# Kernel optimization log

Measured on AMD Instinct MI355X. Metric: run time of the kernel, lower is better.

Reference implementation:

```python
import jax, jax.numpy as jnp
import numpy as np

B, T, E, H = 2, 2048, 1024, 16
D = E // H
K_KEEP = 391
RECENCY = 64
SCALE = D ** -0.5


def setup_inputs() -> dict:
    key = jax.random.key(0)
    k1, k2, k3 = jax.random.split(key, 3)
    x = jax.random.normal(k1, (B, T, E), jnp.float32)
    W_attn = jax.random.normal(k2, (3 * E, E), jnp.float32) * 0.02  # torch Linear weight [out,in]
    W_proj = jax.random.normal(k3, (E, E), jnp.float32) * 0.02
    return {"x": x, "W_attn": W_attn, "W_proj": W_proj}


def reference(x, W_attn, W_proj):
    b, t, c = x.shape
    qkv = x @ W_attn.T                      # [B,T,3E]
    q, k, v = jnp.split(qkv, 3, axis=-1)
    to_heads = lambda u: u.reshape(b, t, H, D).transpose(0, 2, 1, 3)  # [B,H,T,D]
    q, k, v = to_heads(q), to_heads(k), to_heads(v)

    # first pass: causal attention weights for importance scoring
    scores = jnp.einsum('bhqd,bhkd->bhqk', q, k) * SCALE
    causal = jnp.tril(jnp.ones((t, t), dtype=bool))
    scores = jnp.where(causal, scores, -jnp.inf)
    attn_w = jax.nn.softmax(scores, axis=-1)

    # mean importance over query dim, force-keep recent tokens
    imp = attn_w.mean(axis=2)               # [B,H,T]
    imp = imp.at[:, :, -RECENCY:].set(1.0)

    # top-k token selection per (batch, head)
    _, idx = jax.lax.top_k(imp, K_KEEP)     # [B,H,K]

    # gather pruned K/V
    K_keep = jnp.take_along_axis(k, idx[..., None], axis=2)  # [B,H,K,D]
    V_keep = jnp.take_along_axis(v, idx[..., None], axis=2)

    # second attention pass over pruned keys (no causal mask, matches legacy code)
    s2 = jnp.einsum('bhqd,bhkd->bhqk', q, K_keep) * SCALE
    a2 = jax.nn.softmax(s2, axis=-1)
    out = jnp.einsum('bhqk,bhkd->bhqd', a2, V_keep)          # [B,H,T,D]

    out = out.transpose(0, 2, 1, 3).reshape(b, t, c)
    return out @ W_proj.T
```

## Files before the change

kernel.cpp:

```cpp
#include <hip/hip_runtime.h>
#include <hip/hip_bf16.h>


#define TT 2048
#define EE 1024
#define HH 16
#define DD 64
#define KKEEP 391
#define REC 64
#define NBH 32
#define QSCALE 0.125f
#define KPAD 448

typedef short bf16x8 __attribute__((ext_vector_type(8)));
typedef _Float16 f16x8 __attribute__((ext_vector_type(8)));
typedef float f32x4 __attribute__((ext_vector_type(4)));

#define WAIT_VM(N) asm volatile("s_waitcnt vmcnt(" #N ")" ::: "memory")
#define WAIT_LGKM0 asm volatile("s_waitcnt lgkmcnt(0)" ::: "memory")
#define BAR() __builtin_amdgcn_s_barrier()

static __device__ inline unsigned short bf_rn(float x) {
  unsigned u = __float_as_uint(x);
  unsigned r = u + 0x7fffu + ((u >> 16) & 1u);
  return (unsigned short)(r >> 16);
}
static __device__ inline float bf_up(unsigned short h) {
  return __uint_as_float((unsigned)h << 16);
}
static __device__ inline unsigned pkf16(float a, float b) {
  union { _Float16 h[2]; unsigned u; } t;
  t.h[0] = (_Float16)a; t.h[1] = (_Float16)b; return t.u;
}
static __device__ inline void glds16(const void* g, void* l) {
  __builtin_amdgcn_global_load_lds(
      (const __attribute__((address_space(1))) void*)g,
      (__attribute__((address_space(3))) void*)l, 16, 0, 0);
}

static __device__ inline void split4(const float* __restrict__ src,
                                     unsigned short* __restrict__ ho,
                                     unsigned short* __restrict__ lo_, int i)
{
  float4 v = *reinterpret_cast<const float4*>(&src[i]);
  ushort4 hh, ll;
  float f;
  hh.x = bf_rn(v.x); f = bf_up(hh.x); ll.x = bf_rn(v.x - f);
  hh.y = bf_rn(v.y); f = bf_up(hh.y); ll.y = bf_rn(v.y - f);
  hh.z = bf_rn(v.z); f = bf_up(hh.z); ll.z = bf_rn(v.z - f);
  hh.w = bf_rn(v.w); f = bf_up(hh.w); ll.w = bf_rn(v.w - f);
  *reinterpret_cast<ushort4*>(&ho[i]) = hh;
  *reinterpret_cast<ushort4*>(&lo_[i]) = ll;
}

__global__ __launch_bounds__(256) void split_kernel(
    const float* __restrict__ src, unsigned short* __restrict__ ho,
    unsigned short* __restrict__ lo_, int n)
{
  int i = (blockIdx.x * 256 + threadIdx.x) * 4;
  const int stride = gridDim.x * 1024;
  for (; i < n; i += stride) split4(src, ho, lo_, i);
}

__global__ __launch_bounds__(256) void split2_kernel(
    const float* __restrict__ x, const float* __restrict__ wa,
    unsigned short* __restrict__ xh, unsigned short* __restrict__ xl,
    unsigned short* __restrict__ wh, unsigned short* __restrict__ wl)
{
  const int n1 = 4096 * 1024, n2 = 3072 * 1024;
  int i = (blockIdx.x * 256 + threadIdx.x) * 4;
  const int stride = gridDim.x * 1024;
  for (; i < n1 + n2; i += stride) {
    if (i < n1) split4(x, xh, xl, i);
    else        split4(wa, wh, wl, i - n1);
  }
}

template<bool VB, int MODE>
__global__ __launch_bounds__(256) void gemm_pipe(
    const unsigned short* __restrict__ Ah, const unsigned short* __restrict__ Al,
    const unsigned short* __restrict__ Bh, const unsigned short* __restrict__ Bl,
    float* __restrict__ Cc, unsigned short* __restrict__ Qho, unsigned short* __restrict__ Qlo,
    unsigned short* __restrict__ Kho, unsigned short* __restrict__ Klo,
    float* __restrict__ Vo, int M, int N, int Kd, int nOff)
{
  __shared__ __align__(16) unsigned short Ahs[2][128 * 32];
  __shared__ __align__(16) unsigned short Bhs[2][128 * 32];
  __shared__ __align__(16) unsigned short Als[VB ? 1 : 2][128 * 32];
  __shared__ __align__(16) unsigned short Bls[VB ? 1 : 2][128 * 32];
  const int tid = threadIdx.x;
  const int m0 = blockIdx.y * 128, n0 = nOff + blockIdx.x * 128;
  const int w = tid >> 6, lane = tid & 63;
  const int wm = w >> 1, wn = w & 1;
  const int l15 = lane & 15, l4 = lane >> 4;

  size_t gA[2], gB[2]; int ldso[2];
#pragma unroll
  for (int s = 0; s < 2; s++) {
    int seg = w * 2 + s;
    int r = seg * 16 + (lane >> 2);
    int kb = (lane & 3) ^ ((r >> 1) & 3);
    gA[s] = (size_t)(m0 + r) * Kd + kb * 8;
    gB[s] = (size_t)(n0 + r) * Kd + kb * 8;
    ldso[s] = seg * 512;
  }
  auto STAGE = [&](int bb, int k0) {
#pragma unroll
    for (int s = 0; s < 2; s++) {
      glds16(&Ah[gA[s] + k0], &Ahs[bb][ldso[s]]);
      glds16(&Bh[gB[s] + k0], &Bhs[bb][ldso[s]]);
      if (!VB) {
        glds16(&Al[gA[s] + k0], &Als[bb][ldso[s]]);
        glds16(&Bl[gB[s] + k0], &Bls[bb][ldso[s]]);
      }
    }
  };

  f32x4 acc[4][4] = {};

  STAGE(0, 0);
  STAGE(1, 32);
  int cur = 0;
  for (int k0 = 0; k0 < Kd; k0 += 32) {
    if (k0 + 32 < Kd) { if (VB) WAIT_VM(4); else WAIT_VM(8); }
    else WAIT_VM(0);
    BAR();
    bf16x8 ah[4], al[4], bh[4], bl[4];
#pragma unroll
    for (int i = 0; i < 4; i++) {
      int ar = wm * 64 + i * 16 + l15;
      int aoff = ar * 32 + ((l4 ^ ((ar >> 1) & 3)) * 8);
      ah[i] = *reinterpret_cast<const bf16x8*>(&Ahs[cur][aoff]);
      int br = wn * 64 + i * 16 + l15;
      int boff = br * 32 + ((l4 ^ ((br >> 1) & 3)) * 8);
      bh[i] = *reinterpret_cast<const bf16x8*>(&Bhs[cur][boff]);
      if (!VB) {
        al[i] = *reinterpret_cast<const bf16x8*>(&Als[cur][aoff]);
        bl[i] = *reinterpret_cast<const bf16x8*>(&Bls[cur][boff]);
      }
    }
#pragma unroll
    for (int i = 0; i < 4; i++)
#pragma unroll
      for (int j = 0; j < 4; j++) {
        acc[i][j] = __builtin_amdgcn_mfma_f32_16x16x32_bf16(ah[i], bh[j], acc[i][j], 0, 0, 0);
        if (!VB) {
          acc[i][j] = __builtin_amdgcn_mfma_f32_16x16x32_bf16(ah[i], bl[j], acc[i][j], 0, 0, 0);
          acc[i][j] = __builtin_amdgcn_mfma_f32_16x16x32_bf16(al[i], bh[j], acc[i][j], 0, 0, 0);
        }
      }
    WAIT_LGKM0;
    BAR();
    if (k0 + 64 < Kd) STAGE(cur, k0 + 64);
    cur ^= 1;
  }

  if (MODE == 0) {
#pragma unroll
    for (int i = 0; i < 4; i++) {
      int mrow0 = m0 + wm * 64 + i * 16 + l4 * 4;
#pragma unroll
      for (int j = 0; j < 4; j++) {
        int ncol = n0 + wn * 64 + j * 16 + l15;
#pragma unroll
        for (int r = 0; r < 4; r++)
          Cc[(size_t)(mrow0 + r) * N + ncol] = acc[i][j][r];
      }
    }
  } else if (VB) {
#pragma unroll
    for (int j = 0; j < 4; j++) {
      int n = n0 + wn * 64 + j * 16 + l15;
      int rr = n & 1023;
      int h = rr >> 6, d0 = rr & 63;
#pragma unroll
      for (int i = 0; i < 4; i++) {
        int mrow0 = m0 + wm * 64 + i * 16 + l4 * 4;
#pragma unroll
        for (int r = 0; r < 4; r++) {
          int m = mrow0 + r;
          int b = m >> 11, t = m & 2047;
          Vo[((size_t)((b * HH + h) * TT + t)) * DD + d0] = acc[i][j][r];
        }
      }
    }
  } else {
#pragma unroll
    for (int j = 0; j < 4; j++) {
      int n = n0 + wn * 64 + j * 16 + l15;
      int p = n >> 10, rr = n & 1023;
      int h = rr >> 6, d0 = rr & 63;
#pragma unroll
      for (int i = 0; i < 4; i++) {
        int mrow0 = m0 + wm * 64 + i * 16 + l4 * 4;
#pragma unroll
        for (int r = 0; r < 4; r++) {
          int m = mrow0 + r;
          int b = m >> 11, t = m & 2047;
          size_t idx = ((size_t)((b * HH + h) * TT + t)) * DD + d0;
          float v = acc[i][j][r];
          unsigned short hi_ = bf_rn(v);
          unsigned short lo2 = bf_rn(v - bf_up(hi_));
          if (p == 0) { Qho[idx] = hi_; Qlo[idx] = lo2; }
          else        { Kho[idx] = hi_; Klo[idx] = lo2; }
        }
      }
    }
  }
}

__global__ __launch_bounds__(512) void importance4_kernel(
    const unsigned short* __restrict__ Qh, const unsigned short* __restrict__ Ql,
    const unsigned short* __restrict__ Kh, const unsigned short* __restrict__ Kl,
    float* __restrict__ part)
{
  const int pairid = blockIdx.y, bh = blockIdx.x;
  const int tid = threadIdx.x;
  const int w = tid >> 6, lane = tid & 63;
  const int wm = w >> 1, wn = w & 1;
  const int l15 = lane & 15, l4 = lane >> 4;
  __shared__ __align__(16) unsigned short Qhs[128 * 64];
  __shared__ __align__(16) unsigned short Qls[128 * 64];
  __shared__ __align__(16) unsigned short Khs[2][128 * 64];
  __shared__ __align__(16) unsigned short Kls[2][128 * 64];
  __shared__ float csw[8 * 128];
  __shared__ float rsb[2 * 128];

  int krow[2], kkb[2], klds[2];
#pragma unroll
  for (int s = 0; s < 2; s++) {
    int seg = w * 2 + s;
    int r = seg * 8 + (lane >> 3);
    int k8 = lane & 7;
    krow[s] = r; kkb[s] = k8 ^ (r & 7); klds[s] = seg * 512;
  }
  auto STAGEK = [&](int bb, int ci) {
#pragma unroll
    for (int s = 0; s < 2; s++) {
      size_t ga = ((size_t)(bh * TT + ci * 128 + krow[s])) * DD + kkb[s] * 8;
      glds16(&Kh[ga], &Khs[bb][klds[s]]);
      glds16(&Kl[ga], &Kls[bb][klds[s]]);
    }
  };

  for (int half = 0; half < 2; half++) {
    const int rt = half ? (15 - pairid) : pairid;
    const int row0 = rt * 128;
    const int nch = rt + 1;
    __syncthreads();
#pragma unroll
    for (int cc = 0; cc < 2; cc++) {
      int c = cc * 512 + tid;
      int r = c >> 3, k8 = c & 7;
      int so = r * 64 + ((k8 ^ (r & 7)) * 8);
      size_t ga = ((size_t)(bh * TT + row0 + r)) * DD + k8 * 8;
      *reinterpret_cast<bf16x8*>(&Qhs[so]) = *reinterpret_cast<const bf16x8*>(&Qh[ga]);
      *reinterpret_cast<bf16x8*>(&Qls[so]) = *reinterpret_cast<const bf16x8*>(&Ql[ga]);
    }
    __syncthreads();
    bf16x8 aq[2][2], aql[2][2];
#pragma unroll
    for (int ks = 0; ks < 2; ks++)
#pragma unroll
      for (int i = 0; i < 2; i++) {
        int ar = wm * 32 + i * 16 + l15;
        int off = ar * 64 + (((ks * 4 + l4) ^ (ar & 7)) * 8);
        aq[ks][i]  = *reinterpret_cast<const bf16x8*>(&Qhs[off]);
        aql[ks][i] = *reinterpret_cast<const bf16x8*>(&Qls[off]);
      }

    float rsum[2][4];
#pragma unroll
    for (int i = 0; i < 2; i++)
#pragma unroll
      for (int r = 0; r < 4; r++) rsum[i][r] = 0.f;
    float invl[2][4];

    for (int sweep = 0; sweep < 2; sweep++) {
      STAGEK(0, 0);
      if (nch > 1) STAGEK(1, 1);
      int cur = 0;
      for (int ci = 0; ci < nch; ci++) {
        if (ci + 1 < nch) WAIT_VM(4); else WAIT_VM(0);
        BAR();
        f32x4 acc[2][4] = {};
#pragma unroll
        for (int ks = 0; ks < 2; ks++) {
#pragma unroll
          for (int j = 0; j < 4; j++) {
            int br = wn * 64 + j * 16 + l15;
            int off = br * 64 + (((ks * 4 + l4) ^ (br & 7)) * 8);
            bf16x8 bh_ = *reinterpret_cast<const bf16x8*>(&Khs[cur][off]);
            bf16x8 bl_ = *reinterpret_cast<const bf16x8*>(&Kls[cur][off]);
#pragma unroll
            for (int i = 0; i < 2; i++) {
              acc[i][j] = __builtin_amdgcn_mfma_f32_16x16x32_bf16(aq[ks][i], bh_, acc[i][j], 0, 0, 0);
              acc[i][j] = __builtin_amdgcn_mfma_f32_16x16x32_bf16(aq[ks][i], bl_, acc[i][j], 0, 0, 0);
              acc[i][j] = __builtin_amdgcn_mfma_f32_16x16x32_bf16(aql[ks][i], bh_, acc[i][j], 0, 0, 0);
            }
          }
        }
        const bool diag = (ci == rt);
        if (sweep == 0) {
#pragma unroll
          for (int i = 0; i < 2; i++)
#pragma unroll
            for (int r = 0; r < 4; r++) {
              int row = row0 + wm * 32 + i * 16 + l4 * 4 + r;
              float s = 0.f;
#pragma unroll
              for (int j = 0; j < 4; j++) {
                int key = ci * 128 + wn * 64 + j * 16 + l15;
                float p = __expf(acc[i][j][r] * QSCALE);
                if (diag && key > row) p = 0.f;
                s += p;
              }
              rsum[i][r] += s;
            }
          WAIT_LGKM0;
          BAR();
          if (ci + 2 < nch) STAGEK(cur, ci + 2);
        } else {
          float cp[4];
#pragma unroll
          for (int j = 0; j < 4; j++) cp[j] = 0.f;
#pragma unroll
          for (int i = 0; i < 2; i++)
#pragma unroll
            for (int r = 0; r < 4; r++) {
              int row = row0 + wm * 32 + i * 16 + l4 * 4 + r;
              float il = invl[i][r];
#pragma unroll
              for (int j = 0; j < 4; j++) {
                int key = ci * 128 + wn * 64 + j * 16 + l15;
                float p = __expf(acc[i][j][r] * QSCALE) * il;
                if (diag && key > row) p = 0.f;
                cp[j] += p;
              }
            }
#pragma unroll
          for (int j = 0; j < 4; j++) {
            float v = cp[j];
            v += __shfl_xor(v, 16); v += __shfl_xor(v, 32);
            cp[j] = v;
          }
          WAIT_LGKM0;
          BAR();
          if (ci + 2 < nch) STAGEK(cur, ci + 2);
          if (l4 == 0) {
#pragma unroll
            for (int j = 0; j < 4; j++)
              csw[w * 128 + wn * 64 + j * 16 + l15] = cp[j];
          }
          WAIT_LGKM0;
          BAR();
          if (tid < 128) {
            int wnc = tid >> 6;
            float s = csw[(0 * 2 + wnc) * 128 + tid] + csw[(1 * 2 + wnc) * 128 + tid] +
                      csw[(2 * 2 + wnc) * 128 + tid] + csw[(3 * 2 + wnc) * 128 + tid];
            size_t pi = ((size_t)(bh * 8 + pairid)) * 2048 + ci * 128 + tid;
            bool wr = (half == 0) || (ci > pairid);
            part[pi] = wr ? s : (part[pi] + s);
          }
        }
        cur ^= 1;
      }
      if (sweep == 0) {
#pragma unroll
        for (int i = 0; i < 2; i++)
#pragma unroll
          for (int r = 0; r < 4; r++) {
            float v = rsum[i][r];
            v += __shfl_xor(v, 1); v += __shfl_xor(v, 2);
            v += __shfl_xor(v, 4); v += __shfl_xor(v, 8);
            rsum[i][r] = v;
          }
        __syncthreads();
        if (l15 == 0) {
#pragma unroll
          for (int i = 0; i < 2; i++)
#pragma unroll
            for (int r = 0; r < 4; r++)
              rsb[wn * 128 + wm * 32 + i * 16 + l4 * 4 + r] = rsum[i][r];
        }
        __syncthreads();
#pragma unroll
        for (int i = 0; i < 2; i++)
#pragma unroll
          for (int r = 0; r < 4; r++) {
            int rl = wm * 32 + i * 16 + l4 * 4 + r;
            invl[i][r] = 1.0f / (rsb[rl] + rsb[128 + rl]);
          }
      }
    }
  }
}

__global__ __launch_bounds__(256) void topk_gather_kernel(
    const float* __restrict__ part,
    const unsigned short* __restrict__ Kh, const unsigned short* __restrict__ Kl,
    const float* __restrict__ V,
    unsigned short* __restrict__ Kf, unsigned short* __restrict__ Vt)
{
  const int bh = blockIdx.x, tid = threadIdx.x;
  const int lane = tid & 63, w = tid >> 6;
  __shared__ int redi[4];
  __shared__ int stot;
  __shared__ int base[256];
  __shared__ int idxb[KKEEP];
  unsigned u[8];
#pragma unroll
  for (int k = 0; k < 8; k++) {
    int e = tid * 8 + k;
    float s = 0.f;
#pragma unroll
    for (int p = 0; p < 8; p++)
      if (e < (16 - p) * 128) s += part[((size_t)(bh * 8 + p)) * 2048 + e];
    float v = (e >= TT - REC) ? 3.0e3f : s;
    u[k] = __float_as_uint(v);
  }
  unsigned lo = 0u, hi = 0x7f800000u;
  for (int it = 0; it < 31; it++) {
    unsigned mid = lo + ((hi - lo + 1) >> 1);
    int c = 0;
#pragma unroll
    for (int k = 0; k < 8; k++) c += (u[k] >= mid) ? 1 : 0;
#pragma unroll
    for (int off = 1; off <= 32; off <<= 1) c += __shfl_xor(c, off);
    if (lane == 0) redi[w] = c;
    __syncthreads();
    int tot = redi[0] + redi[1] + redi[2] + redi[3];
    if (tot >= KKEEP) lo = mid; else hi = mid - 1;
    __syncthreads();
  }
  const unsigned vstar = lo;
  int cgt = 0, ceq = 0;
#pragma unroll
  for (int k = 0; k < 8; k++) { cgt += (u[k] > vstar) ? 1 : 0; ceq += (u[k] == vstar) ? 1 : 0; }
  base[tid] = cgt; __syncthreads();
  if (tid == 0) {
    int run = 0;
    for (int i = 0; i < 256; i++) { int t = base[i]; base[i] = run; run += t; }
    stot = run;
  }
  __syncthreads();
  int off1 = base[tid];
#pragma unroll
  for (int k = 0; k < 8; k++)
    if (u[k] > vstar) idxb[off1++] = tid * 8 + k;
  __syncthreads();
  base[tid] = ceq; __syncthreads();
  if (tid == 0) {
    int run = 0;
    for (int i = 0; i < 256; i++) { int t = base[i]; base[i] = run; run += t; }
  }
  __syncthreads();
  int off2 = stot + base[tid];
#pragma unroll
  for (int k = 0; k < 8; k++)
    if (u[k] == vstar) { if (off2 < KKEEP) idxb[off2] = tid * 8 + k; off2++; }
  __syncthreads();
  for (int f = tid; f < KPAD * 8; f += 256) {
    int kk = f >> 3, c8 = f & 7;
    union { _Float16 h[8]; uint4 v; } o;
#pragma unroll
    for (int j = 0; j < 8; j++) o.h[j] = (_Float16)0.f;
    if (kk < KKEEP) {
      int sr = idxb[kk];
      bf16x8 hv = *reinterpret_cast<const bf16x8*>(&Kh[((size_t)(bh * TT + sr)) * DD + c8 * 8]);
      bf16x8 lv = *reinterpret_cast<const bf16x8*>(&Kl[((size_t)(bh * TT + sr)) * DD + c8 * 8]);
#pragma unroll
      for (int j = 0; j < 8; j++)
        o.h[j] = (_Float16)(bf_up((unsigned short)hv[j]) + bf_up((unsigned short)lv[j]));
    }
    *reinterpret_cast<uint4*>(&Kf[((size_t)(bh * KPAD) + kk) * DD + c8 * 8]) = o.v;
  }
  for (int f = tid; f < KPAD * 8; f += 256) {
    int kk = f >> 3, d8 = f & 7;
    float vv[8];
#pragma unroll
    for (int j = 0; j < 8; j++) vv[j] = 0.f;
    if (kk < KKEEP) {
      int sr = idxb[kk];
      float4 a = *reinterpret_cast<const float4*>(&V[((size_t)(bh * TT + sr)) * DD + d8 * 8]);
      float4 b = *reinterpret_cast<const float4*>(&V[((size_t)(bh * TT + sr)) * DD + d8 * 8 + 4]);
      vv[0] = a.x; vv[1] = a.y; vv[2] = a.z; vv[3] = a.w;
      vv[4] = b.x; vv[5] = b.y; vv[6] = b.z; vv[7] = b.w;
    }
#pragma unroll
    for (int j = 0; j < 8; j++) {
      union { _Float16 h; unsigned short s; } t;
      t.h = (_Float16)vv[j];
      Vt[((size_t)(bh * DD) + d8 * 8 + j) * KPAD + kk] = t.s;
    }
  }
}

__global__ __launch_bounds__(256) void attn4_kernel(
    const unsigned short* __restrict__ Qh, const unsigned short* __restrict__ Ql,
    const unsigned short* __restrict__ Kf, const unsigned short* __restrict__ Vt,
    unsigned short* __restrict__ AOh, unsigned short* __restrict__ AOl)
{
  const int rt = blockIdx.y, bh = blockIdx.x;
  const int tid = threadIdx.x;
  const int w = tid >> 6, lane = tid & 63;
  const int l15 = lane & 15, l4 = lane >> 4;
  __shared__ __align__(16) unsigned short Qs[64 * 64];
  __shared__ __align__(16) unsigned short Ks[2][64 * 64];
  __shared__ __align__(16) unsigned short Vs[2][64 * 64];
  __shared__ float LDSo[4][64][16];
  const int row0 = rt * 64;

  int srow[2], skb[2], slds[2];
#pragma unroll
  for (int s = 0; s < 2; s++) {
    int seg = w * 2 + s;
    int r = seg * 8 + (lane >> 3);
    int k8 = lane & 7;
    srow[s] = r; skb[s] = k8 ^ (r & 7); slds[s] = seg * 512;
  }
  auto STAGEA = [&](int bb, int ci) {
#pragma unroll
    for (int s = 0; s < 2; s++) {
      glds16(&Kf[((size_t)(bh * KPAD) + ci * 64 + srow[s]) * DD + skb[s] * 8], &Ks[bb][slds[s]]);
      glds16(&Vt[((size_t)(bh * DD) + srow[s]) * KPAD + ci * 64 + skb[s] * 8], &Vs[bb][slds[s]]);
    }
  };

#pragma unroll
  for (int it = 0; it < 2; it++) {
    int idx = it * 256 + tid;
    int r = idx >> 3, k8 = idx & 7;
    size_t ga = ((size_t)(bh * TT + row0 + r)) * DD + k8 * 8;
    bf16x8 hv = *reinterpret_cast<const bf16x8*>(&Qh[ga]);
    bf16x8 lv = *reinterpret_cast<const bf16x8*>(&Ql[ga]);
    union { _Float16 h[8]; uint4 v; } q16;
#pragma unroll
    for (int j = 0; j < 8; j++)
      q16.h[j] = (_Float16)(bf_up((unsigned short)hv[j]) + bf_up((unsigned short)lv[j]));
    *reinterpret_cast<uint4*>(&Qs[r * 64 + ((k8 ^ (r & 7)) * 8)]) = q16.v;
  }
  STAGEA(0, 0);
  STAGEA(1, 1);
  WAIT_LGKM0;
  BAR();
  f16x8 bq[2];
#pragma unroll
  for (int ks = 0; ks < 2; ks++) {
    int br = w * 16 + l15;
    bq[ks] = *reinterpret_cast<const f16x8*>(&Qs[br * 64 + (((ks * 4 + l4) ^ (br & 7)) * 8)]);
  }

  f32x4 acc_o[4] = {};
  float rsum = 0.f;
  int cur = 0;

  for (int ci = 0; ci < 7; ci++) {
    if (ci + 1 < 7) WAIT_VM(4); else WAIT_VM(0);
    BAR();
    f32x4 accs[4] = {};
#pragma unroll
    for (int ks = 0; ks < 2; ks++) {
#pragma unroll
      for (int i = 0; i < 4; i++) {
        int kr = i * 16 + l15;
        f16x8 af = *reinterpret_cast<const f16x8*>(&Ks[cur][kr * 64 + (((ks * 4 + l4) ^ (kr & 7)) * 8)]);
        accs[i] = __builtin_amdgcn_mfma_f32_16x16x32_f16(af, bq[ks], accs[i], 0, 0, 0);
      }
    }
    float p[4][4];
#pragma unroll
    for (int i = 0; i < 4; i++)
#pragma unroll
      for (int r = 0; r < 4; r++) {
        int gk = ci * 64 + i * 16 + l4 * 4 + r;
        float pp = __expf(accs[i][r] * QSCALE);
        if (gk >= KKEEP) pp = 0.f;
        p[i][r] = pp;
        rsum += pp;
      }
    unsigned pkU[4][2];
#pragma unroll
    for (int i = 0; i < 4; i++) {
      pkU[i][0] = pkf16(p[i][0], p[i][1]);
      pkU[i][1] = pkf16(p[i][2], p[i][3]);
    }
#pragma unroll
    for (int ks = 0; ks < 2; ks++) {
      union { f16x8 h; unsigned u[4]; } bp;
#pragma unroll
      for (int wp = 0; wp < 4; wp++) {
        int src = ((l4 & 1) * 2 + (wp >> 1)) * 16 + l15;
        unsigned v0 = (unsigned)__shfl((int)pkU[ks * 2][wp & 1], src);
        unsigned v1 = (unsigned)__shfl((int)pkU[ks * 2 + 1][wp & 1], src);
        bp.u[wp] = (l4 & 2) ? v1 : v0;
      }
#pragma unroll
      for (int i = 0; i < 4; i++) {
        int dr = i * 16 + l15;
        f16x8 av = *reinterpret_cast<const f16x8*>(&Vs[cur][dr * 64 + (((ks * 4 + l4) ^ (dr & 7)) * 8)]);
        acc_o[i] = __builtin_amdgcn_mfma_f32_16x16x32_f16(av, bp.h, acc_o[i], 0, 0, 0);
      }
    }
    WAIT_LGKM0;
    BAR();
    if (ci + 2 < 7) STAGEA(cur, ci + 2);
    cur ^= 1;
  }
  rsum += __shfl_xor(rsum, 16);
  rsum += __shfl_xor(rsum, 32);
  float inv = 1.0f / rsum;
#pragma unroll
  for (int i = 0; i < 4; i++)
#pragma unroll
    for (int r = 0; r < 4; r++)
      LDSo[w][i * 16 + l4 * 4 + r][l15] = acc_o[i][r] * inv;
  __syncthreads();
  const int b = bh >> 4, h = bh & 15;
#pragma unroll
  for (int uu = 0; uu < 2; uu++) {
    int u = uu * 64 + lane;
    int q = u >> 3, dc = u & 7;
    int row = row0 + w * 16 + q;
    union { unsigned short s[8]; uint4 v; } sh, sl;
#pragma unroll
    for (int j = 0; j < 8; j++) {
      float v = LDSo[w][dc * 8 + j][q];
      unsigned short hh = bf_rn(v);
      sh.s[j] = hh;
      sl.s[j] = bf_rn(v - bf_up(hh));
    }
    size_t addr = ((size_t)(b * TT + row)) * EE + h * DD + dc * 8;
    *reinterpret_cast<uint4*>(&AOh[addr]) = sh.v;
    *reinterpret_cast<uint4*>(&AOl[addr]) = sl.v;
  }
}

extern "C" void kernel_launch(void* const* d_in, const int* in_sizes, int n_in,
                              void* d_out, int out_size, void* d_ws, size_t ws_size,
                              hipStream_t stream)
{
  const float* x     = (const float*)d_in[0];
  const float* Wattn = (const float*)d_in[1];
  const float* Wproj = (const float*)d_in[2];
  float* out = (float*)d_out;
  float* ws  = (float*)d_ws;

  const size_t SZQ = (size_t)NBH * TT * DD;
  const size_t SZK = (size_t)NBH * KPAD * DD;
  float* Vb   = ws;
  float* part = Vb + SZQ;
  unsigned short* Kf  = (unsigned short*)(part + (size_t)NBH * 8 * TT);
  unsigned short* Vt  = Kf + SZK;
  unsigned short* Qhp = Vt + SZK;
  unsigned short* Qlp = Qhp + SZQ;
  unsigned short* Khp = Qlp + SZQ;
  unsigned short* Klp = Khp + SZQ;
  unsigned short* xh  = Klp + SZQ;
  unsigned short* xl  = xh + (size_t)4096 * 1024;
  unsigned short* Wh  = xl + (size_t)4096 * 1024;
  unsigned short* Wl  = Wh + (size_t)3072 * 1024;
  unsigned short* AOh = xh;
  unsigned short* AOl = xl;
  unsigned short* Ph  = Wh;
  unsigned short* Pl  = Ph + (size_t)1024 * 1024;

  const size_t needB =
      ((size_t)SZQ + (size_t)NBH * 8 * TT) * 4 +
      ((size_t)2 * SZK + (size_t)4 * SZQ + (size_t)2 * 4096 * 1024 + (size_t)2 * 3072 * 1024) * 2;
  if (ws_size < needB) return;

  split2_kernel<<<1024, 256, 0, stream>>>(x, Wattn, xh, xl, Wh, Wl);
  gemm_pipe<false, 1><<<dim3(16, 32), 256, 0, stream>>>(xh, xl, Wh, Wl, nullptr,
      Qhp, Qlp, Khp, Klp, nullptr, 4096, 3072, 1024, 0);
  gemm_pipe<true, 1><<<dim3(8, 32), 256, 0, stream>>>(xh, xl, Wh, Wl, nullptr,
      nullptr, nullptr, nullptr, nullptr, Vb, 4096, 3072, 1024, 2048);
  split_kernel<<<256, 256, 0, stream>>>(Wproj, Ph, Pl, 1024 * 1024);
  importance4_kernel<<<dim3(NBH, 8), 512, 0, stream>>>(Qhp, Qlp, Khp, Klp, part);
  topk_gather_kernel<<<NBH, 256, 0, stream>>>(part, Khp, Klp, Vb, Kf, Vt);
  attn4_kernel<<<dim3(NBH, 32), 256, 0, stream>>>(Qhp, Qlp, Kf, Vt, AOh, AOl);
  gemm_pipe<false, 0><<<dim3(8, 32), 256, 0, stream>>>(AOh, AOl, Ph, Pl, out,
      nullptr, nullptr, nullptr, nullptr, nullptr, 4096, 1024, 1024, 0);
}
```

Before: 265.0 us.

## Split importance blocks per row tile and use hi-only K in normalizer sweep

The importance kernel now launches one block per 128-row query tile instead of one per balanced tile pair, doubling the grid to 512 blocks. Each block writes its own partial column-sum slab, and top-k sums 16 slabs instead of 8. Q fragments are loaded directly from global memory rather than staged through LDS. The first (row-sum) sweep now uses a single bf16 hi×hi MFMA and stages only Kh. This aims to raise occupancy and cut MFMA and load work, at the cost of less accurate softmax normalizers and a bigger partial buffer.

Result: no change. 261.9 us (-1.2%).

```diff
diff --git a/kernel.cpp b/kernel.cpp
--- a/kernel.cpp
+++ b/kernel.cpp
@@ -209,18 +209,20 @@
   }
 }
 
-__global__ __launch_bounds__(512) void importance4_kernel(
+__global__ __launch_bounds__(512) void importance5_kernel(
     const unsigned short* __restrict__ Qh, const unsigned short* __restrict__ Ql,
     const unsigned short* __restrict__ Kh, const unsigned short* __restrict__ Kl,
     float* __restrict__ part)
 {
-  const int pairid = blockIdx.y, bh = blockIdx.x;
+  const int bh = blockIdx.x;
+  const int rt = blockIdx.z ? (15 - (int)blockIdx.y) : (int)blockIdx.y;
+  const int slab = ((int)blockIdx.y << 1) | (int)blockIdx.z;
+  const int row0 = rt * 128;
+  const int nch = rt + 1;
   const int tid = threadIdx.x;
   const int w = tid >> 6, lane = tid & 63;
   const int wm = w >> 1, wn = w & 1;
   const int l15 = lane & 15, l4 = lane >> 4;
-  __shared__ __align__(16) unsigned short Qhs[128 * 64];
-  __shared__ __align__(16) unsigned short Qls[128 * 64];
   __shared__ __align__(16) unsigned short Khs[2][128 * 64];
   __shared__ __align__(16) unsigned short Kls[2][128 * 64];
   __shared__ float csw[8 * 128];
@@ -234,7 +236,14 @@
     int k8 = lane & 7;
     krow[s] = r; kkb[s] = k8 ^ (r & 7); klds[s] = seg * 512;
   }
-  auto STAGEK = [&](int bb, int ci) {
+  auto STAGEK1 = [&](int bb, int ci) {
+#pragma unroll
+    for (int s = 0; s < 2; s++) {
+      size_t ga = ((size_t)(bh * TT + ci * 128 + krow[s])) * DD + kkb[s] * 8;
+      glds16(&Kh[ga], &Khs[bb][klds[s]]);
+    }
+  };
+  auto STAGEK2 = [&](int bb, int ci) {
 #pragma unroll
     for (int s = 0; s < 2; s++) {
       size_t ga = ((size_t)(bh * TT + ci * 128 + krow[s])) * DD + kkb[s] * 8;
@@ -243,156 +252,154 @@
     }
   };
 
-  for (int half = 0; half < 2; half++) {
-    const int rt = half ? (15 - pairid) : pairid;
-    const int row0 = rt * 128;
-    const int nch = rt + 1;
-    __syncthreads();
-#pragma unroll
-    for (int cc = 0; cc < 2; cc++) {
-      int c = cc * 512 + tid;
-      int r = c >> 3, k8 = c & 7;
-      int so = r * 64 + ((k8 ^ (r & 7)) * 8);
-      size_t ga = ((size_t)(bh * TT + row0 + r)) * DD + k8 * 8;
-      *reinterpret_cast<bf16x8*>(&Qhs[so]) = *reinterpret_cast<const bf16x8*>(&Qh[ga]);
-      *reinterpret_cast<bf16x8*>(&Qls[so]) = *reinterpret_cast<const bf16x8*>(&Ql[ga]);
-    }
-    __syncthreads();
-    bf16x8 aq[2][2], aql[2][2];
-#pragma unroll
-    for (int ks = 0; ks < 2; ks++)
-#pragma unroll
-      for (int i = 0; i < 2; i++) {
-        int ar = wm * 32 + i * 16 + l15;
-        int off = ar * 64 + (((ks * 4 + l4) ^ (ar & 7)) * 8);
-        aq[ks][i]  = *reinterpret_cast<const bf16x8*>(&Qhs[off]);
-        aql[ks][i] = *reinterpret_cast<const bf16x8*>(&Qls[off]);
-      }
-
-    float rsum[2][4];
+  bf16x8 aq[2][2], aql[2][2];
+#pragma unroll
+  for (int ks = 0; ks < 2; ks++)
+#pragma unroll
+    for (int i = 0; i < 2; i++) {
+      int ar = wm * 32 + i * 16 + l15;
+      size_t ga = ((size_t)(bh * TT + row0 + ar)) * DD + (ks * 4 + l4) * 8;
+      aq[ks][i]  = *reinterpret_cast<const bf16x8*>(&Qh[ga]);
+      aql[ks][i] = *reinterpret_cast<const bf16x8*>(&Ql[ga]);
+    }
+
+  float rsum[2][4];
+#pragma unroll
+  for (int i = 0; i < 2; i++)
+#pragma unroll
+    for (int r = 0; r < 4; r++) rsum[i][r] = 0.f;
+  float invl[2][4];
+
+  STAGEK1(0, 0);
+  if (nch > 1) STAGEK1(1, 1);
+  int cur = 0;
+  for (int ci = 0; ci < nch; ci++) {
+    if (ci + 1 < nch) WAIT_VM(2); else WAIT_VM(0);
+    BAR();
+    f32x4 acc[2][4] = {};
+#pragma unroll
+    for (int ks = 0; ks < 2; ks++) {
+#pragma unroll
+      for (int j = 0; j < 4; j++) {
+        int br = wn * 64 + j * 16 + l15;
+        int off = br * 64 + (((ks * 4 + l4) ^ (br & 7)) * 8);
+        bf16x8 bh_ = *reinterpret_cast<const bf16x8*>(&Khs[cur][off]);
+#pragma unroll
+        for (int i = 0; i < 2; i++)
+          acc[i][j] = __builtin_amdgcn_mfma_f32_16x16x32_bf16(aq[ks][i], bh_, acc[i][j], 0, 0, 0);
+      }
+    }
+    const bool diag = (ci == rt);
 #pragma unroll
     for (int i = 0; i < 2; i++)
 #pragma unroll
-      for (int r = 0; r < 4; r++) rsum[i][r] = 0.f;
-    float invl[2][4];
-
-    for (int sweep = 0; sweep < 2; sweep++) {
-      STAGEK(0, 0);
-      if (nch > 1) STAGEK(1, 1);
-      int cur = 0;
-      for (int ci = 0; ci < nch; ci++) {
-        if (ci + 1 < nch) WAIT_VM(4); else WAIT_VM(0);
-        BAR();
-        f32x4 acc[2][4] = {};
-#pragma unroll
-        for (int ks = 0; ks < 2; ks++) {
-#pragma unroll
-          for (int j = 0; j < 4; j++) {
-            int br = wn * 64 + j * 16 + l15;
-            int off = br * 64 + (((ks * 4 + l4) ^ (br & 7)) * 8);
-            bf16x8 bh_ = *reinterpret_cast<const bf16x8*>(&Khs[cur][off]);
-            bf16x8 bl_ = *reinterpret_cast<const bf16x8*>(&Kls[cur][off]);
-#pragma unroll
-            for (int i = 0; i < 2; i++) {
-              acc[i][j] = __builtin_amdgcn_mfma_f32_16x16x32_bf16(aq[ks][i], bh_, acc[i][j], 0, 0, 0);
-              acc[i][j] = __builtin_amdgcn_mfma_f32_16x16x32_bf16(aq[ks][i], bl_, acc[i][j], 0, 0, 0);
-              acc[i][j] = __builtin_amdgcn_mfma_f32_16x16x32_bf16(aql[ks][i], bh_, acc[i][j], 0, 0, 0);
-            }
-          }
+      for (int r = 0; r < 4; r++) {
+        int row = row0 + wm * 32 + i * 16 + l4 * 4 + r;
+        float s = 0.f;
+#pragma unroll
+        for (int j = 0; j < 4; j++) {
+          int key = ci * 128 + wn * 64 + j * 16 + l15;
+          float p = __expf(acc[i][j][r] * QSCALE);
+          if (diag && key > row) p = 0.f;
+          s += p;
         }
-        const bool diag = (ci == rt);
-        if (sweep == 0) {
-#pragma unroll
-          for (int i = 0; i < 2; i++)
-#pragma unroll
-            for (int r = 0; r < 4; r++) {
-              int row = row0 + wm * 32 + i * 16 + l4 * 4 + r;
-              float s = 0.f;
-#pragma unroll
-              for (int j = 0; j < 4; j++) {
-                int key = ci * 128 + wn * 64 + j * 16 + l15;
-                float p = __expf(acc[i][j][r] * QSCALE);
-                if (diag && key > row) p = 0.f;
-                s += p;
-              }
-              rsum[i][r] += s;
-            }
-          WAIT_LGKM0;
-          BAR();
-          if (ci + 2 < nch) STAGEK(cur, ci + 2);
-        } else {
-          float cp[4];
-#pragma unroll
-          for (int j = 0; j < 4; j++) cp[j] = 0.f;
-#pragma unroll
-          for (int i = 0; i < 2; i++)
-#pragma unroll
-            for (int r = 0; r < 4; r++) {
-              int row = row0 + wm * 32 + i * 16 + l4 * 4 + r;
-              float il = invl[i][r];
-#pragma unroll
-              for (int j = 0; j < 4; j++) {
-                int key = ci * 128 + wn * 64 + j * 16 + l15;
-                float p = __expf(acc[i][j][r] * QSCALE) * il;
-                if (diag && key > row) p = 0.f;
-                cp[j] += p;
-              }
-            }
-#pragma unroll
-          for (int j = 0; j < 4; j++) {
-            float v = cp[j];
-            v += __shfl_xor(v, 16); v += __shfl_xor(v, 32);
-            cp[j] = v;
-          }
-          WAIT_LGKM0;
-          BAR();
-          if (ci + 2 < nch) STAGEK(cur, ci + 2);
-          if (l4 == 0) {
-#pragma unroll
-            for (int j = 0; j < 4; j++)
-              csw[w * 128 + wn * 64 + j * 16 + l15] = cp[j];
-          }
-          WAIT_LGKM0;
-          BAR();
-          if (tid < 128) {
-            int wnc = tid >> 6;
-            float s = csw[(0 * 2 + wnc) * 128 + tid] + csw[(1 * 2 + wnc) * 128 + tid] +
-                      csw[(2 * 2 + wnc) * 128 + tid] + csw[(3 * 2 + wnc) * 128 + tid];
-            size_t pi = ((size_t)(bh * 8 + pairid)) * 2048 + ci * 128 + tid;
-            bool wr = (half == 0) || (ci > pairid);
-            part[pi] = wr ? s : (part[pi] + s);
-          }
+        rsum[i][r] += s;
+      }
+    WAIT_LGKM0;
+    BAR();
+    if (ci + 2 < nch) STAGEK1(cur, ci + 2);
+    cur ^= 1;
+  }
+#pragma unroll
+  for (int i = 0; i < 2; i++)
+#pragma unroll
+    for (int r = 0; r < 4; r++) {
+      float v = rsum[i][r];
+      v += __shfl_xor(v, 1); v += __shfl_xor(v, 2);
+      v += __shfl_xor(v, 4); v += __shfl_xor(v, 8);
+      rsum[i][r] = v;
+    }
+  __syncthreads();
+  if (l15 == 0) {
+#pragma unroll
+    for (int i = 0; i < 2; i++)
+#pragma unroll
+      for (int r = 0; r < 4; r++)
+        rsb[wn * 128 + wm * 32 + i * 16 + l4 * 4 + r] = rsum[i][r];
+  }
+  __syncthreads();
+#pragma unroll
+  for (int i = 0; i < 2; i++)
+#pragma unroll
+    for (int r = 0; r < 4; r++) {
+      int rl = wm * 32 + i * 16 + l4 * 4 + r;
+      invl[i][r] = 1.0f / (rsb[rl] + rsb[128 + rl]);
+    }
+
+  STAGEK2(0, 0);
+  if (nch > 1) STAGEK2(1, 1);
+  cur = 0;
+  for (int ci = 0; ci < nch; ci++) {
+    if (ci + 1 < nch) WAIT_VM(4); else WAIT_VM(0);
+    BAR();
+    f32x4 acc[2][4] = {};
+#pragma unroll
+    for (int ks = 0; ks < 2; ks++) {
+#pragma unroll
+      for (int j = 0; j < 4; j++) {
+        int br = wn * 64 + j * 16 + l15;
+        int off = br * 64 + (((ks * 4 + l4) ^ (br & 7)) * 8);
+        bf16x8 bh_ = *reinterpret_cast<const bf16x8*>(&Khs[cur][off]);
+        bf16x8 bl_ = *reinterpret_cast<const bf16x8*>(&Kls[cur][off]);
+#pragma unroll
+        for (int i = 0; i < 2; i++) {
+          acc[i][j] = __builtin_amdgcn_mfma_f32_16x16x32_bf16(aq[ks][i], bh_, acc[i][j], 0, 0, 0);
+          acc[i][j] = __builtin_amdgcn_mfma_f32_16x16x32_bf16(aq[ks][i], bl_, acc[i][j], 0, 0, 0);
+          acc[i][j] = __builtin_amdgcn_mfma_f32_16x16x32_bf16(aql[ks][i], bh_, acc[i][j], 0, 0, 0);
         }
-        cur ^= 1;
-      }
-      if (sweep == 0) {
-#pragma unroll
-        for (int i = 0; i < 2; i++)
-#pragma unroll
-          for (int r = 0; r < 4; r++) {
-            float v = rsum[i][r];
-            v += __shfl_xor(v, 1); v += __shfl_xor(v, 2);
-            v += __shfl_xor(v, 4); v += __shfl_xor(v, 8);
-            rsum[i][r] = v;
-          }
-        __syncthreads();
-        if (l15 == 0) {
-#pragma unroll
-          for (int i = 0; i < 2; i++)
-#pragma unroll
-            for (int r = 0; r < 4; r++)
-              rsb[wn * 128 + wm * 32 + i * 16 + l4 * 4 + r] = rsum[i][r];
+      }
+    }
+    const bool diag = (ci == rt);
+    float cp[4];
+#pragma unroll
+    for (int j = 0; j < 4; j++) cp[j] = 0.f;
+#pragma unroll
+    for (int i = 0; i < 2; i++)
+#pragma unroll
+      for (int r = 0; r < 4; r++) {
+        int row = row0 + wm * 32 + i * 16 + l4 * 4 + r;
+        float il = invl[i][r];
+#pragma unroll
+        for (int j = 0; j < 4; j++) {
+          int key = ci * 128 + wn * 64 + j * 16 + l15;
+          float p = __expf(acc[i][j][r] * QSCALE) * il;
+          if (diag && key > row) p = 0.f;
+          cp[j] += p;
         }
-        __syncthreads();
-#pragma unroll
-        for (int i = 0; i < 2; i++)
-#pragma unroll
-          for (int r = 0; r < 4; r++) {
-            int rl = wm * 32 + i * 16 + l4 * 4 + r;
-            invl[i][r] = 1.0f / (rsb[rl] + rsb[128 + rl]);
-          }
-      }
-    }
+      }
+#pragma unroll
+    for (int j = 0; j < 4; j++) {
+      float v = cp[j];
+      v += __shfl_xor(v, 16); v += __shfl_xor(v, 32);
+      cp[j] = v;
+    }
+    WAIT_LGKM0;
+    BAR();
+    if (ci + 2 < nch) STAGEK2(cur, ci + 2);
+    if (l4 == 0) {
+#pragma unroll
+      for (int j = 0; j < 4; j++)
+        csw[w * 128 + wn * 64 + j * 16 + l15] = cp[j];
+    }
+    WAIT_LGKM0;
+    BAR();
+    if (tid < 128) {
+      int wnc = tid >> 6;
+      float s = csw[(0 * 2 + wnc) * 128 + tid] + csw[(1 * 2 + wnc) * 128 + tid] +
+                csw[(2 * 2 + wnc) * 128 + tid] + csw[(3 * 2 + wnc) * 128 + tid];
+      part[((size_t)(bh * 16 + slab)) * 2048 + ci * 128 + tid] = s;
+    }
+    cur ^= 1;
   }
 }
 
@@ -414,8 +421,10 @@
     int e = tid * 8 + k;
     float s = 0.f;
 #pragma unroll
-    for (int p = 0; p < 8; p++)
-      if (e < (16 - p) * 128) s += part[((size_t)(bh * 8 + p)) * 2048 + e];
+    for (int p = 0; p < 16; p++) {
+      int rtp = (p & 1) ? 15 - (p >> 1) : (p >> 1);
+      if (e < (rtp + 1) * 128) s += part[((size_t)(bh * 16 + p)) * 2048 + e];
+    }
     float v = (e >= TT - REC) ? 3.0e3f : s;
     u[k] = __float_as_uint(v);
   }
@@ -650,7 +659,7 @@
   const size_t SZK = (size_t)NBH * KPAD * DD;
   float* Vb   = ws;
   float* part = Vb + SZQ;
-  unsigned short* Kf  = (unsigned short*)(part + (size_t)NBH * 8 * TT);
+  unsigned short* Kf  = (unsigned short*)(part + (size_t)NBH * 16 * TT);
   unsigned short* Vt  = Kf + SZK;
   unsigned short* Qhp = Vt + SZK;
   unsigned short* Qlp = Qhp + SZQ;
@@ -666,7 +675,7 @@
   unsigned short* Pl  = Ph + (size_t)1024 * 1024;
 
   const size_t needB =
-      ((size_t)SZQ + (size_t)NBH * 8 * TT) * 4 +
+      ((size_t)SZQ + (size_t)NBH * 16 * TT) * 4 +
       ((size_t)2 * SZK + (size_t)4 * SZQ + (size_t)2 * 4096 * 1024 + (size_t)2 * 3072 * 1024) * 2;
   if (ws_size < needB) return;
 
@@ -676,7 +685,7 @@
   gemm_pipe<true, 1><<<dim3(8, 32), 256, 0, stream>>>(xh, xl, Wh, Wl, nullptr,
       nullptr, nullptr, nullptr, nullptr, Vb, 4096, 3072, 1024, 2048);
   split_kernel<<<256, 256, 0, stream>>>(Wproj, Ph, Pl, 1024 * 1024);
-  importance4_kernel<<<dim3(NBH, 8), 512, 0, stream>>>(Qhp, Qlp, Khp, Klp, part);
+  importance5_kernel<<<dim3(NBH, 8, 2), 512, 0, stream>>>(Qhp, Qlp, Khp, Klp, part);
   topk_gather_kernel<<<NBH, 256, 0, stream>>>(part, Khp, Klp, Vb, Kf, Vt);
   attn4_kernel<<<dim3(NBH, 32), 256, 0, stream>>>(Qhp, Qlp, Kf, Vt, AOh, AOl);
   gemm_pipe<false, 0><<<dim3(8, 32), 256, 0, stream>>>(AOh, AOl, Ph, Pl, out,
```
